# Kernel tuning notes

Measured on AMD Instinct MI355X. Metric: run time of the kernel, lower is better.

Reference implementation:

```python
import jax, jax.numpy as jnp
import numpy as np

N, E, D, K, NCONV = 50000, 800000, 64, 3, 6


def setup_inputs() -> dict:
    key = jax.random.key(0)
    ks = jax.random.split(key, 6)
    X = jax.random.normal(ks[0], (N, D), jnp.float32)
    edge_index = jax.random.randint(ks[1], (2, E), 0, N, dtype=jnp.int64)
    edge_weight = jax.random.uniform(ks[2], (E,), jnp.float32)
    H = jax.random.normal(ks[3], (N, D), jnp.float32)
    lambda_max = jnp.ones((1,), jnp.float32) * 2.0  # typical sym-normalized Laplacian bound
    conv_w = jax.random.normal(ks[4], (NCONV, K, D, D), jnp.float32) / np.sqrt(D)
    conv_b = jnp.zeros((NCONV, D), jnp.float32)
    return {"X": X, "edge_index": edge_index, "edge_weight": edge_weight,
            "H": H, "lambda_max": lambda_max, "conv_w": conv_w, "conv_b": conv_b}


def reference(X, edge_index, edge_weight, H, lambda_max, conv_w, conv_b):
    src, dst = edge_index[0], edge_index[1]
    # symmetric normalization: norm_e = w_e / sqrt(deg_src * deg_dst)
    deg = jax.ops.segment_sum(edge_weight, src, num_segments=N)
    dinv = jnp.where(deg > 0, deg ** -0.5, 0.0)
    norm = edge_weight * dinv[src] * dinv[dst]  # [E]
    lam = lambda_max.reshape(())
    c = 2.0 / lam

    def a_prop(v):  # A_norm @ v via scatter-add over edges, [N,D]
        return jax.ops.segment_sum(norm[:, None] * v[src], dst, num_segments=N)

    def l_hat(v):  # (2/lam)(I - A_norm) v - v
        return (c - 1.0) * v - c * a_prop(v)

    def cheb(v, w, b):  # ChebConv order K: sum_k T_k(L_hat) v @ W_k + b
        tx0, tx1 = v, l_hat(v)
        out = tx0 @ w[0] + tx1 @ w[1]
        for k in range(2, K):
            tx2 = 2.0 * l_hat(tx1) - tx0
            out = out + tx2 @ w[k]
            tx0, tx1 = tx1, tx2
        return out + b

    Z = jax.nn.sigmoid(cheb(X, conv_w[0], conv_b[0]) + cheb(H, conv_w[1], conv_b[1]))
    R = jax.nn.sigmoid(cheb(X, conv_w[2], conv_b[2]) + cheb(H, conv_w[3], conv_b[3]))
    H_tilde = jnp.tanh(cheb(X, conv_w[4], conv_b[4]) + cheb(H * R, conv_w[5], conv_b[5]))
    return Z * H_tilde + (1.0 - Z) * H
```

## Files before the change

### kernel.cpp

```cpp
#include <hip/hip_runtime.h>
#include <cstdint>
#include <cstddef>

typedef unsigned int u32;
typedef unsigned short u16;
typedef unsigned long long u64;

#define D 64
#define CAP 5120
#define CPAD 16
#define CEMAX 2048

typedef __attribute__((ext_vector_type(8))) short bf16x8;
typedef __attribute__((ext_vector_type(4))) float f32x4;

static __device__ __forceinline__ float sigmoidf_(float x) {
    return 1.f / (1.f + __expf(-x));
}
static __device__ __forceinline__ u16 f2bf(float x) {
    u32 u = __float_as_uint(x);
    return (u16)((u + 0x7fffu + ((u >> 16) & 1u)) >> 16);
}
static __device__ __forceinline__ u32 packbf2(float a, float b) {
    return (u32)f2bf(a) | ((u32)f2bf(b) << 16);
}
static __device__ __forceinline__ float bflo(u32 u) { return __uint_as_float(u << 16); }
static __device__ __forceinline__ float bfhi(u32 u) { return __uint_as_float(u & 0xffff0000u); }


__global__ void init_kernel(u32* cur_d, u32* cur_s) {
    int t = threadIdx.x;
    cur_d[t * CPAD] = (u32)(t * CAP);
    cur_s[t * CPAD] = (u32)(t * CAP);
}

__global__ __launch_bounds__(256) void coarse_prep_kernel(
    const int* __restrict__ src, const int* __restrict__ dst, const float* __restrict__ w,
    u32* cur_d, u32* cur_s,
    u64* __restrict__ slab_d, u32* __restrict__ slab_s,
    const float* __restrict__ X, const float* __restrict__ Hf,
    const float* __restrict__ convw,
    u32* __restrict__ XH_t, u32* __restrict__ WT,
    int E, int CE, int nch, int total) {
    __shared__ __align__(16) char smem[CEMAX * 12 + 6 * 1024 + 64];
    int t = threadIdx.x;
    int blk = blockIdx.x;

    if (blk >= nch) {
        int pb = blk - nch;
        if (pb < 18) {
            float (*s)[68] = (float (*)[68])smem;
            const float* wp = convw + (size_t)pb * 4096;
            for (int i = t; i < 1024; i += 256) {
                int k = i >> 4, c4 = (i & 15) * 4;
                *(float4*)&s[k][c4] = *(const float4*)&wp[k * 64 + c4];
            }
            __syncthreads();
            for (int i = t; i < 2048; i += 256) {
                int uk = i & 31, nn = i >> 5;
                WT[(size_t)pb * 2048 + nn * 32 + uk] = packbf2(s[2 * uk][nn], s[2 * uk + 1][nn]);
            }
            return;
        }
        int i = (pb - 18) * 256 + t;
        if (i >= total) return;
        int nn = i >> 6, l = i & 63;
        const float* sp = (l < 32 ? X : Hf) + (size_t)nn * 64 + ((2 * l) & 63);
        float2 v = *(const float2*)sp;
        XH_t[i] = packbf2(v.x, v.y);
        return;
    }

    u64* st_d = (u64*)smem;
    u32* st_s = (u32*)(smem + CEMAX * 8);
    u32* hd = (u32*)(smem + CEMAX * 12);
    u32* hs = hd + 256;
    u32* bd = hs + 256;
    u32* bs = bd + 256;
    u32* gd = bs + 256;
    u32* gs = gd + 256;
    u32* wsd = gs + 256;
    u32* wss = wsd + 4;
    int c = blk;
    hd[t] = 0; hs[t] = 0;
    __syncthreads();
    int e0 = c * CE, e1 = min(E, e0 + CE);
    int m = e1 - e0;
    for (int e = e0 + t; e < e1; e += 256) {
        atomicAdd(&hd[(u32)dst[e] >> 8], 1u);
        atomicAdd(&hs[(u32)src[e] >> 8], 1u);
    }
    __syncthreads();
    u32 vd = hd[t], vs = hs[t];
    u32 id = vd, is_ = vs;
    int lane = t & 63, wv = t >> 6;
#pragma unroll
    for (int o = 1; o < 64; o <<= 1) {
        u32 xd = __shfl_up(id, o, 64);
        u32 xs = __shfl_up(is_, o, 64);
        if (lane >= o) { id += xd; is_ += xs; }
    }
    if (lane == 63) { wsd[wv] = id; wss[wv] = is_; }
    __syncthreads();
    u32 addd = 0, adds = 0;
    for (int i = 0; i < wv; ++i) { addd += wsd[i]; adds += wss[i]; }
    id += addd; is_ += adds;
    u32 exd = id - vd, exs = is_ - vs;
    gd[t] = atomicAdd(&cur_d[t * CPAD], vd);
    gs[t] = atomicAdd(&cur_s[t * CPAD], vs);
    bd[t] = exd; bs[t] = exs;
    hd[t] = exd; hs[t] = exs;
    __syncthreads();
    for (int e = e0 + t; e < e1; e += 256) {
        int s = src[e], d = dst[e];
        float wf = w[e];
        u32 pbd = (u32)d >> 8, pbs = (u32)s >> 8;
        u32 pd = atomicAdd(&hd[pbd], 1u);
        u32 ps = atomicAdd(&hs[pbs], 1u);
        st_d[pd] = (u64)((u32)s | (((u32)d & 255u) << 16) | (pbd << 24)) |
                   ((u64)__float_as_uint(wf) << 32);
        st_s[ps] = ((u32)s & 255u) | (pbs << 8) | ((u32)f2bf(wf) << 16);
    }
    __syncthreads();
    for (int i = t; i < m; i += 256) {
        u64 r = st_d[i];
        u32 b = (u32)(r >> 24) & 255u;
        u32 gpos = gd[b] + ((u32)i - bd[b]);
        if (gpos < (b + 1u) * CAP) slab_d[gpos] = r;
    }
    for (int i = t; i < m; i += 256) {
        u32 r = st_s[i];
        u32 b = (r >> 8) & 255u;
        u32 gpos = gs[b] + ((u32)i - bs[b]);
        if (gpos < (b + 1u) * CAP) slab_s[gpos] = r;
    }
}

__global__ __launch_bounds__(256) void fine_fused_kernel(
    const u64* __restrict__ slab_d, const u32* __restrict__ slab_s,
    const u32* __restrict__ cur_d, const u32* __restrict__ cur_s,
    float* __restrict__ dinv, u32* __restrict__ edge4,
    int2* __restrict__ rowinfo, int NB, int N_) {
    int t = threadIdx.x;
    int b = blockIdx.x;
    if (b < NB) {
        __shared__ float dg[256];
        int m = min((int)cur_s[b * CPAD] - b * CAP, CAP);
        const u32* rp = slab_s + (size_t)b * CAP;
        dg[t] = 0.f;
        __syncthreads();
        for (int i = t; i < m; i += 256) {
            u32 r = rp[i];
            atomicAdd(&dg[r & 255u], __uint_as_float(r & 0xffff0000u));
        }
        __syncthreads();
        int node = (b << 8) + t;
        if (node < N_) dinv[node] = (dg[t] > 0.f) ? rsqrtf(dg[t]) : 0.f;
        return;
    }
    b -= NB;
    __shared__ int h[256], cur[256], ws[4];
    int m = min((int)cur_d[b * CPAD] - b * CAP, CAP);
    const u64* rp = slab_d + (size_t)b * CAP;
    h[t] = 0;
    __syncthreads();
    for (int i = t; i < m; i += 256) atomicAdd(&h[(int)((rp[i] >> 16) & 255u)], 1);
    __syncthreads();
    int v = h[t];
    int iv = v;
    int lane = t & 63, wv = t >> 6;
#pragma unroll
    for (int o = 1; o < 64; o <<= 1) {
        int x = __shfl_up(iv, o, 64);
        if (lane >= o) iv += x;
    }
    if (lane == 63) ws[wv] = iv;
    __syncthreads();
    int add = 0;
    for (int i = 0; i < wv; ++i) add += ws[i];
    iv += add;
    int excl = iv - v;
    cur[t] = excl;
    int bs = b * CAP;
    int node = (b << 8) + t;
    if (node < N_) rowinfo[node] = make_int2(bs + excl, v);
    __syncthreads();
    for (int i = t; i < m; i += 256) {
        u64 r = rp[i];
        int f = (int)((r >> 16) & 255u);
        int p = atomicAdd(&cur[f], 1);
        u32 sidx = (u32)(r & 0xffffu);
        float wf = __uint_as_float((u32)(r >> 32));
        edge4[bs + p] = sidx | ((u32)f2bf(wf) << 16);
    }
}


__global__ __launch_bounds__(256) void lhat128_kernel(
    const u32* __restrict__ vt, const u32* __restrict__ w0t,
    u32* __restrict__ out_t,
    const int2* __restrict__ rowinfo, const float* __restrict__ dinv,
    const u32* __restrict__ edges, const float* __restrict__ lam_ptr, int n) {
    int node = (blockIdx.x * blockDim.x + threadIdx.x) >> 6;
    if (node >= n) return;
    int l = threadIdx.x & 63;
    int g = l >> 4, f = l & 15;
    int2 ri = rowinfo[node];
    int e0 = ri.x, end = e0 + ri.y;
    float acc[8];
#pragma unroll
    for (int j = 0; j < 8; j++) acc[j] = 0.f;

    int base = e0;
    for (; base + 16 <= end; base += 16) {
        u32 r0 = edges[base + g];
        u32 r1 = edges[base + 4 + g];
        u32 r2 = edges[base + 8 + g];
        u32 r3 = edges[base + 12 + g];
        float d0 = dinv[r0 & 0xffffu];
        float d1 = dinv[r1 & 0xffffu];
        float d2 = dinv[r2 & 0xffffu];
        float d3 = dinv[r3 & 0xffffu];
        const uint4 q0 = *(const uint4*)(vt + (size_t)(r0 & 0xffffu) * 64 + 4 * f);
        const uint4 q1 = *(const uint4*)(vt + (size_t)(r1 & 0xffffu) * 64 + 4 * f);
        const uint4 q2 = *(const uint4*)(vt + (size_t)(r2 & 0xffffu) * 64 + 4 * f);
        const uint4 q3 = *(const uint4*)(vt + (size_t)(r3 & 0xffffu) * 64 + 4 * f);
        float n0 = __uint_as_float(r0 & 0xffff0000u) * d0;
        float n1 = __uint_as_float(r1 & 0xffff0000u) * d1;
        float n2 = __uint_as_float(r2 & 0xffff0000u) * d2;
        float n3 = __uint_as_float(r3 & 0xffff0000u) * d3;
        acc[0] += n0 * bflo(q0.x); acc[1] += n0 * bfhi(q0.x);
        acc[2] += n0 * bflo(q0.y); acc[3] += n0 * bfhi(q0.y);
        acc[4] += n0 * bflo(q0.z); acc[5] += n0 * bfhi(q0.z);
        acc[6] += n0 * bflo(q0.w); acc[7] += n0 * bfhi(q0.w);
        acc[0] += n1 * bflo(q1.x); acc[1] += n1 * bfhi(q1.x);
        acc[2] += n1 * bflo(q1.y); acc[3] += n1 * bfhi(q1.y);
        acc[4] += n1 * bflo(q1.z); acc[5] += n1 * bfhi(q1.z);
        acc[6] += n1 * bflo(q1.w); acc[7] += n1 * bfhi(q1.w);
        acc[0] += n2 * bflo(q2.x); acc[1] += n2 * bfhi(q2.x);
        acc[2] += n2 * bflo(q2.y); acc[3] += n2 * bfhi(q2.y);
        acc[4] += n2 * bflo(q2.z); acc[5] += n2 * bfhi(q2.z);
        acc[6] += n2 * bflo(q2.w); acc[7] += n2 * bfhi(q2.w);
        acc[0] += n3 * bflo(q3.x); acc[1] += n3 * bfhi(q3.x);
        acc[2] += n3 * bflo(q3.y); acc[3] += n3 * bfhi(q3.y);
        acc[4] += n3 * bflo(q3.z); acc[5] += n3 * bfhi(q3.z);
        acc[6] += n3 * bflo(q3.w); acc[7] += n3 * bfhi(q3.w);
    }
    for (; base < end; base += 4) {
        int ei = base + g;
        u32 r0 = (ei < end) ? edges[ei] : 0u;
        float d0 = dinv[r0 & 0xffffu];
        const uint4 q0 = *(const uint4*)(vt + (size_t)(r0 & 0xffffu) * 64 + 4 * f);
        float n0 = __uint_as_float(r0 & 0xffff0000u) * d0;
        acc[0] += n0 * bflo(q0.x); acc[1] += n0 * bfhi(q0.x);
        acc[2] += n0 * bflo(q0.y); acc[3] += n0 * bfhi(q0.y);
        acc[4] += n0 * bflo(q0.z); acc[5] += n0 * bfhi(q0.z);
        acc[6] += n0 * bflo(q0.w); acc[7] += n0 * bfhi(q0.w);
    }
#pragma unroll
    for (int m = 16; m <= 32; m <<= 1)
#pragma unroll
        for (int j = 0; j < 8; j++) acc[j] += __shfl_xor(acc[j], m);

    const uint4 sv = *(const uint4*)(vt + (size_t)node * 64 + 4 * f);
    float self[8];
    self[0] = bflo(sv.x); self[1] = bfhi(sv.x);
    self[2] = bflo(sv.y); self[3] = bfhi(sv.y);
    self[4] = bflo(sv.z); self[5] = bfhi(sv.z);
    self[6] = bflo(sv.w); self[7] = bfhi(sv.w);
    float c = 2.f / lam_ptr[0];
    float dv = dinv[node];
    float rx[8];
#pragma unroll
    for (int j = 0; j < 8; j++) rx[j] = (c - 1.f) * self[j] - (c * dv) * acc[j];
    if (w0t) {
        const uint4 wv4 = *(const uint4*)(w0t + (size_t)node * 64 + 4 * f);
        rx[0] = 2.f * rx[0] - bflo(wv4.x); rx[1] = 2.f * rx[1] - bfhi(wv4.x);
        rx[2] = 2.f * rx[2] - bflo(wv4.y); rx[3] = 2.f * rx[3] - bfhi(wv4.y);
        rx[4] = 2.f * rx[4] - bflo(wv4.z); rx[5] = 2.f * rx[5] - bfhi(wv4.z);
        rx[6] = 2.f * rx[6] - bflo(wv4.w); rx[7] = 2.f * rx[7] - bfhi(wv4.w);
    }
    if (l < 16) {
        uint4 o;
        o.x = packbf2(rx[0], rx[1]); o.y = packbf2(rx[2], rx[3]);
        o.z = packbf2(rx[4], rx[5]); o.w = packbf2(rx[6], rx[7]);
        *(uint4*)(out_t + (size_t)node * 64 + 4 * f) = o;
    }
}

__global__ __launch_bounds__(256) void lhat64_kernel(
    const u32* __restrict__ vt, const u32* __restrict__ w0t,
    u32* __restrict__ out_t,
    const int2* __restrict__ rowinfo, const float* __restrict__ dinv,
    const u32* __restrict__ edges, const float* __restrict__ lam_ptr, int n) {
    int node = (blockIdx.x * blockDim.x + threadIdx.x) >> 6;
    if (node >= n) return;
    int l = threadIdx.x & 63;
    int g = l >> 3, f = l & 7;
    int2 ri = rowinfo[node];
    int e0 = ri.x, end = e0 + ri.y;
    float acc[8];
#pragma unroll
    for (int j = 0; j < 8; j++) acc[j] = 0.f;

    int base = e0;
    for (; base + 16 <= end; base += 16) {
        u32 r0 = edges[base + g];
        u32 r1 = edges[base + 8 + g];
        float d0 = dinv[r0 & 0xffffu];
        float d1 = dinv[r1 & 0xffffu];
        const uint4 q0 = *(const uint4*)(vt + (size_t)(r0 & 0xffffu) * 32 + 4 * f);
        const uint4 q1 = *(const uint4*)(vt + (size_t)(r1 & 0xffffu) * 32 + 4 * f);
        float n0 = __uint_as_float(r0 & 0xffff0000u) * d0;
        float n1 = __uint_as_float(r1 & 0xffff0000u) * d1;
        acc[0] += n0 * bflo(q0.x); acc[1] += n0 * bfhi(q0.x);
        acc[2] += n0 * bflo(q0.y); acc[3] += n0 * bfhi(q0.y);
        acc[4] += n0 * bflo(q0.z); acc[5] += n0 * bfhi(q0.z);
        acc[6] += n0 * bflo(q0.w); acc[7] += n0 * bfhi(q0.w);
        acc[0] += n1 * bflo(q1.x); acc[1] += n1 * bfhi(q1.x);
        acc[2] += n1 * bflo(q1.y); acc[3] += n1 * bfhi(q1.y);
        acc[4] += n1 * bflo(q1.z); acc[5] += n1 * bfhi(q1.z);
        acc[6] += n1 * bflo(q1.w); acc[7] += n1 * bfhi(q1.w);
    }
    for (; base < end; base += 8) {
        int ei = base + g;
        u32 r0 = (ei < end) ? edges[ei] : 0u;
        float d0 = dinv[r0 & 0xffffu];
        const uint4 q0 = *(const uint4*)(vt + (size_t)(r0 & 0xffffu) * 32 + 4 * f);
        float n0 = __uint_as_float(r0 & 0xffff0000u) * d0;
        acc[0] += n0 * bflo(q0.x); acc[1] += n0 * bfhi(q0.x);
        acc[2] += n0 * bflo(q0.y); acc[3] += n0 * bfhi(q0.y);
        acc[4] += n0 * bflo(q0.z); acc[5] += n0 * bfhi(q0.z);
        acc[6] += n0 * bflo(q0.w); acc[7] += n0 * bfhi(q0.w);
    }
#pragma unroll
    for (int m = 8; m <= 32; m <<= 1)
#pragma unroll
        for (int j = 0; j < 8; j++) acc[j] += __shfl_xor(acc[j], m);

    const uint4 sv = *(const uint4*)(vt + (size_t)node * 32 + 4 * f);
    float self[8];
    self[0] = bflo(sv.x); self[1] = bfhi(sv.x);
    self[2] = bflo(sv.y); self[3] = bfhi(sv.y);
    self[4] = bflo(sv.z); self[5] = bfhi(sv.z);
    self[6] = bflo(sv.w); self[7] = bfhi(sv.w);
    float c = 2.f / lam_ptr[0];
    float dv = dinv[node];
    float rx[8];
#pragma unroll
    for (int j = 0; j < 8; j++) rx[j] = (c - 1.f) * self[j] - (c * dv) * acc[j];
    if (w0t) {
        const uint4 wv4 = *(const uint4*)(w0t + (size_t)node * 32 + 4 * f);
        rx[0] = 2.f * rx[0] - bflo(wv4.x); rx[1] = 2.f * rx[1] - bfhi(wv4.x);
        rx[2] = 2.f * rx[2] - bflo(wv4.y); rx[3] = 2.f * rx[3] - bfhi(wv4.y);
        rx[4] = 2.f * rx[4] - bflo(wv4.z); rx[5] = 2.f * rx[5] - bfhi(wv4.z);
        rx[6] = 2.f * rx[6] - bflo(wv4.w); rx[7] = 2.f * rx[7] - bfhi(wv4.w);
    }
    if (l < 8) {
        uint4 o;
        o.x = packbf2(rx[0], rx[1]); o.y = packbf2(rx[2], rx[3]);
        o.z = packbf2(rx[4], rx[5]); o.w = packbf2(rx[6], rx[7]);
        *(uint4*)(out_t + (size_t)node * 32 + 4 * f) = o;
    }
}

__global__ __launch_bounds__(512) void gemm_gate_kernel(
    const u32* __restrict__ A0, const u32* __restrict__ A1, const u32* __restrict__ A2,
    const u32* __restrict__ WT, const float* __restrict__ convb,
    const float* __restrict__ Hf,
    float* __restrict__ Zb, float* __restrict__ Sh,
    u16* __restrict__ HR_t, int n) {
    __shared__ u32 Ws[64 * 36];
    int t = threadIdx.x;
    int wv = t >> 6, l = t & 63;
    int q = l >> 4, ml = l & 15;
    int R = blockIdx.x * 128 + wv * 16;
    int ar = R + ml; if (ar >= n) ar = n - 1;

    f32x4 S[3][4];
#pragma unroll
    for (int tg = 0; tg < 3; tg++)
#pragma unroll
        for (int ni = 0; ni < 4; ni++) S[tg][ni] = (f32x4){0.f, 0.f, 0.f, 0.f};

    for (int kt = 0; kt < 3; kt++) {
        const u32* Ap = (kt == 0) ? A0 : ((kt == 1) ? A1 : A2);
        const u32* ap = Ap + (size_t)ar * 64 + q * 4;
        bf16x8 af[2][2];
        af[0][0] = *(const bf16x8*)(ap +  0);
        af[1][0] = *(const bf16x8*)(ap + 16);
        af[0][1] = *(const bf16x8*)(ap + 32);
        af[1][1] = *(const bf16x8*)(ap + 48);
#pragma unroll
        for (int cg = 0; cg < 5; cg++) {
            int hf = cg & 1, tg = cg >> 1;
            const u32* Wp = WT + (size_t)(cg * 3 + kt) * 2048;
            __syncthreads();
            {
                int i0 = t * 4;
                uint4 w0 = *(const uint4*)(Wp + i0);
                *(uint4*)&Ws[(i0 >> 5) * 36 + (i0 & 31)] = w0;
            }
            __syncthreads();
#pragma unroll
            for (int h = 0; h < 2; h++) {
                bf16x8 bw[4];
#pragma unroll
                for (int ni = 0; ni < 4; ni++)
                    bw[ni] = *(const bf16x8*)&Ws[(ni * 16 + ml) * 36 + q * 4 + h * 16];
#pragma unroll
                for (int ni = 0; ni < 4; ni++)
                    S[tg][ni] = __builtin_amdgcn_mfma_f32_16x16x32_bf16(
                        af[h][hf], bw[ni], S[tg][ni], 0, 0, 0);
            }
        }
    }
#pragma unroll
    for (int ni = 0; ni < 4; ni++) {
        int col = ni * 16 + ml;
        float bz = convb[col] + convb[64 + col];
        float br = convb[128 + col] + convb[192 + col];
#pragma unroll
        for (int reg = 0; reg < 4; reg++) {
            int row = R + q * 4 + reg;
            if (row < n) {
                size_t o = (size_t)row * 64 + col;
                float z = sigmoidf_(S[0][ni][reg] + bz);
                float r = sigmoidf_(S[1][ni][reg] + br);
                float hr = Hf[o] * r;
                Zb[o] = z;
                Sh[o] = S[2][ni][reg];
                HR_t[o] = f2bf(hr);
            }
        }
    }
}

__global__ __launch_bounds__(512) void gemm_final_kernel(
    const u32* __restrict__ A0, const u32* __restrict__ A1, const u32* __restrict__ A2,
    const u32* __restrict__ WT, const float* __restrict__ convb,
    const float* __restrict__ Zb, const float* __restrict__ Sh, const float* __restrict__ Hf,
    float* __restrict__ outp, int n) {
    __shared__ u32 Ws[64 * 36];
    int t = threadIdx.x;
    int wv = t >> 6, l = t & 63;
    int q = l >> 4, ml = l & 15;
    int R = blockIdx.x * 128 + wv * 16;
    int ar = R + ml; if (ar >= n) ar = n - 1;

    f32x4 S[4];
#pragma unroll
    for (int ni = 0; ni < 4; ni++) S[ni] = (f32x4){0.f, 0.f, 0.f, 0.f};

    for (int kt = 0; kt < 3; kt++) {
        const u32* Ap = (kt == 0) ? A0 : ((kt == 1) ? A1 : A2);
        const u32* ap = Ap + (size_t)ar * 32 + q * 4;
        bf16x8 af[2];
        af[0] = *(const bf16x8*)(ap +  0);
        af[1] = *(const bf16x8*)(ap + 16);
        const u32* Wp = WT + (size_t)(15 + kt) * 2048;
        __syncthreads();
        {
            int i0 = t * 4;
            uint4 w0 = *(const uint4*)(Wp + i0);
            *(uint4*)&Ws[(i0 >> 5) * 36 + (i0 & 31)] = w0;
        }
        __syncthreads();
#pragma unroll
        for (int h = 0; h < 2; h++) {
            bf16x8 bw[4];
#pragma unroll
            for (int ni = 0; ni < 4; ni++)
                bw[ni] = *(const bf16x8*)&Ws[(ni * 16 + ml) * 36 + q * 4 + h * 16];
#pragma unroll
            for (int ni = 0; ni < 4; ni++)
                S[ni] = __builtin_amdgcn_mfma_f32_16x16x32_bf16(af[h], bw[ni], S[ni], 0, 0, 0);
        }
    }
#pragma unroll
    for (int ni = 0; ni < 4; ni++) {
        int col = ni * 16 + ml;
        float bh = convb[256 + col] + convb[320 + col];
#pragma unroll
        for (int reg = 0; reg < 4; reg++) {
            int row = R + q * 4 + reg;
            if (row < n) {
                size_t o = (size_t)row * 64 + col;
                float z = Zb[o];
                float ht = tanhf(S[ni][reg] + Sh[o] + bh);
                outp[o] = z * ht + (1.f - z) * Hf[o];
            }
        }
    }
}


extern "C" void kernel_launch(void* const* d_in, const int* in_sizes, int n_in,
                              void* d_out, int out_size, void* d_ws, size_t ws_size,
                              hipStream_t stream) {
    const float* X     = (const float*)d_in[0];
    const int*   ei    = (const int*)d_in[1];
    const float* ew    = (const float*)d_in[2];
    const float* H     = (const float*)d_in[3];
    const float* lam   = (const float*)d_in[4];
    const float* convw = (const float*)d_in[5];
    const float* convb = (const float*)d_in[6];
    float* out = (float*)d_out;

    const int N = in_sizes[0] / D;
    const int E = in_sizes[2];
    const int* src = ei;
    const int* dst = ei + E;

    const int NB = (N + 255) >> 8;
    const int nch = (E + CEMAX - 1) / CEMAX;
    const int CE = (E + nch - 1) / nch;

    char* p = (char*)d_ws;
    auto alloc = [&](size_t bytes) {
        void* r = (void*)p;
        p += (bytes + 255) & ~(size_t)255;
        return r;
    };
    float* Zb   = (float*)alloc((size_t)N * 64 * 4);
    float* Sh   = (float*)alloc((size_t)N * 64 * 4);
    u32* XH_t = (u32*)alloc((size_t)N * 64 * 4);
    u32* T1_t = (u32*)alloc((size_t)N * 64 * 4);
    u32* T2_t = (u32*)alloc((size_t)N * 64 * 4);
    u16* HR_t = (u16*)alloc((size_t)N * 64 * 2);
    u16* U1_t = (u16*)alloc((size_t)N * 64 * 2);
    u16* U2_t = (u16*)alloc((size_t)N * 64 * 2);
    u32* edge4 = (u32*)alloc((size_t)NB * CAP * 4);
    u64* slab_d = (u64*)alloc((size_t)NB * CAP * 8);
    u32* slab_s = (u32*)alloc((size_t)NB * CAP * 4);
    u32* cur_d  = (u32*)alloc(256 * CPAD * 4);
    u32* cur_s  = (u32*)alloc(256 * CPAD * 4);
    int2* rowinfo  = (int2*)alloc((size_t)N * 8);
    float* dinv    = (float*)alloc((size_t)N * 4);
    u32* WT = (u32*)alloc((size_t)18 * 2048 * 4);

    const int BLK = 256;
    const int gND  = (N * D + BLK - 1) / BLK;
    const int gWav = gND;
    const int gx128 = (N + 127) / 128;

    init_kernel<<<1, 256, 0, stream>>>(cur_d, cur_s);
    coarse_prep_kernel<<<nch + 18 + gND, BLK, 0, stream>>>(
        src, dst, ew, cur_d, cur_s, slab_d, slab_s,
        X, H, convw, XH_t, WT, E, CE, nch, N * D);
    fine_fused_kernel<<<2 * NB, BLK, 0, stream>>>(slab_d, slab_s, cur_d, cur_s,
                                                  dinv, edge4, rowinfo, NB, N);

    lhat128_kernel<<<gWav, BLK, 0, stream>>>(XH_t, nullptr, T1_t,
                                             rowinfo, dinv, edge4, lam, N);
    lhat128_kernel<<<gWav, BLK, 0, stream>>>(T1_t, XH_t, T2_t,
                                             rowinfo, dinv, edge4, lam, N);

    gemm_gate_kernel<<<gx128, 512, 0, stream>>>(XH_t, T1_t, T2_t, WT, convb, H,
                                                Zb, Sh, HR_t, N);

    lhat64_kernel<<<gWav, BLK, 0, stream>>>((const u32*)HR_t, nullptr, (u32*)U1_t,
                                            rowinfo, dinv, edge4, lam, N);
    lhat64_kernel<<<gWav, BLK, 0, stream>>>((const u32*)U1_t, (const u32*)HR_t, (u32*)U2_t,
                                            rowinfo, dinv, edge4, lam, N);

    gemm_final_kernel<<<gx128, 512, 0, stream>>>((const u32*)HR_t, (const u32*)U1_t, (const u32*)U2_t,
                                                 WT, convb, Zb, Sh, H, out, N);
}
```

Before: 280.1 us.

## Fuse second Chebyshev propagation into the GEMM kernels via shared-memory staging

The second L_hat propagation (T2 and U2) is now computed inside the gate and final GEMM kernels, one wave per 16 nodes, with results written to shared memory instead of global buffers. This removes two kernel launches and the global write and read of the T2/U2 intermediates. In exchange, each 512-thread block performs a serial per-node gather before its MFMA phase, on far fewer blocks (N/128). That lowers the parallelism available to hide the gather latency and raises shared-memory use per block.

```diff
diff --git a/kernel.cpp b/kernel.cpp
--- a/kernel.cpp
+++ b/kernel.cpp
@@ -195,22 +195,16 @@
     }
 }
 
-
-__global__ __launch_bounds__(256) void lhat128_kernel(
+static __device__ __forceinline__ void lhat128_body(
     const u32* __restrict__ vt, const u32* __restrict__ w0t,
-    u32* __restrict__ out_t,
     const int2* __restrict__ rowinfo, const float* __restrict__ dinv,
-    const u32* __restrict__ edges, const float* __restrict__ lam_ptr, int n) {
-    int node = (blockIdx.x * blockDim.x + threadIdx.x) >> 6;
-    if (node >= n) return;
-    int l = threadIdx.x & 63;
+    const u32* __restrict__ edges, float c, int node, int l, float rx[8]) {
     int g = l >> 4, f = l & 15;
     int2 ri = rowinfo[node];
     int e0 = ri.x, end = e0 + ri.y;
     float acc[8];
 #pragma unroll
     for (int j = 0; j < 8; j++) acc[j] = 0.f;
-
     int base = e0;
     for (; base + 16 <= end; base += 16) {
         u32 r0 = edges[base + g];
@@ -261,18 +255,13 @@
     for (int m = 16; m <= 32; m <<= 1)
 #pragma unroll
         for (int j = 0; j < 8; j++) acc[j] += __shfl_xor(acc[j], m);
-
     const uint4 sv = *(const uint4*)(vt + (size_t)node * 64 + 4 * f);
-    float self[8];
-    self[0] = bflo(sv.x); self[1] = bfhi(sv.x);
-    self[2] = bflo(sv.y); self[3] = bfhi(sv.y);
-    self[4] = bflo(sv.z); self[5] = bfhi(sv.z);
-    self[6] = bflo(sv.w); self[7] = bfhi(sv.w);
-    float c = 2.f / lam_ptr[0];
     float dv = dinv[node];
-    float rx[8];
-#pragma unroll
-    for (int j = 0; j < 8; j++) rx[j] = (c - 1.f) * self[j] - (c * dv) * acc[j];
+#pragma unroll
+    for (int j = 0; j < 8; j++) {
+        float self = (j & 1) ? bfhi(((const u32*)&sv)[j >> 1]) : bflo(((const u32*)&sv)[j >> 1]);
+        rx[j] = (c - 1.f) * self - (c * dv) * acc[j];
+    }
     if (w0t) {
         const uint4 wv4 = *(const uint4*)(w0t + (size_t)node * 64 + 4 * f);
         rx[0] = 2.f * rx[0] - bflo(wv4.x); rx[1] = 2.f * rx[1] - bfhi(wv4.x);
@@ -280,29 +269,18 @@
         rx[4] = 2.f * rx[4] - bflo(wv4.z); rx[5] = 2.f * rx[5] - bfhi(wv4.z);
         rx[6] = 2.f * rx[6] - bflo(wv4.w); rx[7] = 2.f * rx[7] - bfhi(wv4.w);
     }
-    if (l < 16) {
-        uint4 o;
-        o.x = packbf2(rx[0], rx[1]); o.y = packbf2(rx[2], rx[3]);
-        o.z = packbf2(rx[4], rx[5]); o.w = packbf2(rx[6], rx[7]);
-        *(uint4*)(out_t + (size_t)node * 64 + 4 * f) = o;
-    }
-}
-
-__global__ __launch_bounds__(256) void lhat64_kernel(
+}
+
+static __device__ __forceinline__ void lhat64_body(
     const u32* __restrict__ vt, const u32* __restrict__ w0t,
-    u32* __restrict__ out_t,
     const int2* __restrict__ rowinfo, const float* __restrict__ dinv,
-    const u32* __restrict__ edges, const float* __restrict__ lam_ptr, int n) {
-    int node = (blockIdx.x * blockDim.x + threadIdx.x) >> 6;
-    if (node >= n) return;
-    int l = threadIdx.x & 63;
+    const u32* __restrict__ edges, float c, int node, int l, float rx[8]) {
     int g = l >> 3, f = l & 7;
     int2 ri = rowinfo[node];
     int e0 = ri.x, end = e0 + ri.y;
     float acc[8];
 #pragma unroll
     for (int j = 0; j < 8; j++) acc[j] = 0.f;
-
     int base = e0;
     for (; base + 16 <= end; base += 16) {
         u32 r0 = edges[base + g];
@@ -337,18 +315,13 @@
     for (int m = 8; m <= 32; m <<= 1)
 #pragma unroll
         for (int j = 0; j < 8; j++) acc[j] += __shfl_xor(acc[j], m);
-
     const uint4 sv = *(const uint4*)(vt + (size_t)node * 32 + 4 * f);
-    float self[8];
-    self[0] = bflo(sv.x); self[1] = bfhi(sv.x);
-    self[2] = bflo(sv.y); self[3] = bfhi(sv.y);
-    self[4] = bflo(sv.z); self[5] = bfhi(sv.z);
-    self[6] = bflo(sv.w); self[7] = bfhi(sv.w);
-    float c = 2.f / lam_ptr[0];
     float dv = dinv[node];
-    float rx[8];
-#pragma unroll
-    for (int j = 0; j < 8; j++) rx[j] = (c - 1.f) * self[j] - (c * dv) * acc[j];
+#pragma unroll
+    for (int j = 0; j < 8; j++) {
+        float self = (j & 1) ? bfhi(((const u32*)&sv)[j >> 1]) : bflo(((const u32*)&sv)[j >> 1]);
+        rx[j] = (c - 1.f) * self - (c * dv) * acc[j];
+    }
     if (w0t) {
         const uint4 wv4 = *(const uint4*)(w0t + (size_t)node * 32 + 4 * f);
         rx[0] = 2.f * rx[0] - bflo(wv4.x); rx[1] = 2.f * rx[1] - bfhi(wv4.x);
@@ -356,7 +329,42 @@
         rx[4] = 2.f * rx[4] - bflo(wv4.z); rx[5] = 2.f * rx[5] - bfhi(wv4.z);
         rx[6] = 2.f * rx[6] - bflo(wv4.w); rx[7] = 2.f * rx[7] - bfhi(wv4.w);
     }
+}
+
+
+__global__ __launch_bounds__(256) void lhat128_kernel(
+    const u32* __restrict__ vt, const u32* __restrict__ w0t,
+    u32* __restrict__ out_t,
+    const int2* __restrict__ rowinfo, const float* __restrict__ dinv,
+    const u32* __restrict__ edges, const float* __restrict__ lam_ptr, int n) {
+    int node = (blockIdx.x * blockDim.x + threadIdx.x) >> 6;
+    if (node >= n) return;
+    int l = threadIdx.x & 63;
+    float c = 2.f / lam_ptr[0];
+    float rx[8];
+    lhat128_body(vt, w0t, rowinfo, dinv, edges, c, node, l, rx);
+    if (l < 16) {
+        int f = l;
+        uint4 o;
+        o.x = packbf2(rx[0], rx[1]); o.y = packbf2(rx[2], rx[3]);
+        o.z = packbf2(rx[4], rx[5]); o.w = packbf2(rx[6], rx[7]);
+        *(uint4*)(out_t + (size_t)node * 64 + 4 * f) = o;
+    }
+}
+
+__global__ __launch_bounds__(256) void lhat64_kernel(
+    const u32* __restrict__ vt, const u32* __restrict__ w0t,
+    u32* __restrict__ out_t,
+    const int2* __restrict__ rowinfo, const float* __restrict__ dinv,
+    const u32* __restrict__ edges, const float* __restrict__ lam_ptr, int n) {
+    int node = (blockIdx.x * blockDim.x + threadIdx.x) >> 6;
+    if (node >= n) return;
+    int l = threadIdx.x & 63;
+    float c = 2.f / lam_ptr[0];
+    float rx[8];
+    lhat64_body(vt, w0t, rowinfo, dinv, edges, c, node, l, rx);
     if (l < 8) {
+        int f = l;
         uint4 o;
         o.x = packbf2(rx[0], rx[1]); o.y = packbf2(rx[2], rx[3]);
         o.z = packbf2(rx[4], rx[5]); o.w = packbf2(rx[6], rx[7]);
@@ -364,18 +372,41 @@
     }
 }
 
-__global__ __launch_bounds__(512) void gemm_gate_kernel(
-    const u32* __restrict__ A0, const u32* __restrict__ A1, const u32* __restrict__ A2,
+__global__ __launch_bounds__(512) void lhat_gemm_gate_kernel(
+    const u32* __restrict__ T1, const u32* __restrict__ XH,
+    const int2* __restrict__ rowinfo, const float* __restrict__ dinv,
+    const u32* __restrict__ edges, const float* __restrict__ lam_ptr,
     const u32* __restrict__ WT, const float* __restrict__ convb,
     const float* __restrict__ Hf,
     float* __restrict__ Zb, float* __restrict__ Sh,
     u16* __restrict__ HR_t, int n) {
+    __shared__ u32 T2s[128 * 68];
     __shared__ u32 Ws[64 * 36];
     int t = threadIdx.x;
     int wv = t >> 6, l = t & 63;
+    int R0 = blockIdx.x * 128;
+    float c = 2.f / lam_ptr[0];
+
+    for (int k = 0; k < 16; ++k) {
+        int lr = wv * 16 + k;
+        int node = R0 + lr;
+        if (node < n) {
+            float rx[8];
+            lhat128_body(T1, XH, rowinfo, dinv, edges, c, node, l, rx);
+            if (l < 16) {
+                uint4 o;
+                o.x = packbf2(rx[0], rx[1]); o.y = packbf2(rx[2], rx[3]);
+                o.z = packbf2(rx[4], rx[5]); o.w = packbf2(rx[6], rx[7]);
+                *(uint4*)&T2s[lr * 68 + 4 * l] = o;
+            }
+        }
+    }
+    __syncthreads();
+
     int q = l >> 4, ml = l & 15;
-    int R = blockIdx.x * 128 + wv * 16;
+    int R = R0 + wv * 16;
     int ar = R + ml; if (ar >= n) ar = n - 1;
+    int alr = ar - R0;
 
     f32x4 S[3][4];
 #pragma unroll
@@ -384,13 +415,21 @@
         for (int ni = 0; ni < 4; ni++) S[tg][ni] = (f32x4){0.f, 0.f, 0.f, 0.f};
 
     for (int kt = 0; kt < 3; kt++) {
-        const u32* Ap = (kt == 0) ? A0 : ((kt == 1) ? A1 : A2);
-        const u32* ap = Ap + (size_t)ar * 64 + q * 4;
         bf16x8 af[2][2];
-        af[0][0] = *(const bf16x8*)(ap +  0);
-        af[1][0] = *(const bf16x8*)(ap + 16);
-        af[0][1] = *(const bf16x8*)(ap + 32);
-        af[1][1] = *(const bf16x8*)(ap + 48);
+        if (kt < 2) {
+            const u32* Ap = (kt == 0) ? XH : T1;
+            const u32* ap = Ap + (size_t)ar * 64 + q * 4;
+            af[0][0] = *(const bf16x8*)(ap +  0);
+            af[1][0] = *(const bf16x8*)(ap + 16);
+            af[0][1] = *(const bf16x8*)(ap + 32);
+            af[1][1] = *(const bf16x8*)(ap + 48);
+        } else {
+            const u32* ap = &T2s[alr * 68 + q * 4];
+            af[0][0] = *(const bf16x8*)(ap +  0);
+            af[1][0] = *(const bf16x8*)(ap + 16);
+            af[0][1] = *(const bf16x8*)(ap + 32);
+            af[1][1] = *(const bf16x8*)(ap + 48);
+        }
 #pragma unroll
         for (int cg = 0; cg < 5; cg++) {
             int hf = cg & 1, tg = cg >> 1;
@@ -436,28 +475,57 @@
     }
 }
 
-__global__ __launch_bounds__(512) void gemm_final_kernel(
-    const u32* __restrict__ A0, const u32* __restrict__ A1, const u32* __restrict__ A2,
+__global__ __launch_bounds__(512) void lhat_gemm_final_kernel(
+    const u32* __restrict__ U1, const u32* __restrict__ HR,
+    const int2* __restrict__ rowinfo, const float* __restrict__ dinv,
+    const u32* __restrict__ edges, const float* __restrict__ lam_ptr,
     const u32* __restrict__ WT, const float* __restrict__ convb,
     const float* __restrict__ Zb, const float* __restrict__ Sh, const float* __restrict__ Hf,
     float* __restrict__ outp, int n) {
+    __shared__ u32 U2s[128 * 36];
     __shared__ u32 Ws[64 * 36];
     int t = threadIdx.x;
     int wv = t >> 6, l = t & 63;
+    int R0 = blockIdx.x * 128;
+    float c = 2.f / lam_ptr[0];
+
+    for (int k = 0; k < 16; ++k) {
+        int lr = wv * 16 + k;
+        int node = R0 + lr;
+        if (node < n) {
+            float rx[8];
+            lhat64_body(U1, HR, rowinfo, dinv, edges, c, node, l, rx);
+            if (l < 8) {
+                uint4 o;
+                o.x = packbf2(rx[0], rx[1]); o.y = packbf2(rx[2], rx[3]);
+                o.z = packbf2(rx[4], rx[5]); o.w = packbf2(rx[6], rx[7]);
+                *(uint4*)&U2s[lr * 36 + 4 * l] = o;
+            }
+        }
+    }
+    __syncthreads();
+
     int q = l >> 4, ml = l & 15;
-    int R = blockIdx.x * 128 + wv * 16;
+    int R = R0 + wv * 16;
     int ar = R + ml; if (ar >= n) ar = n - 1;
+    int alr = ar - R0;
 
     f32x4 S[4];
 #pragma unroll
     for (int ni = 0; ni < 4; ni++) S[ni] = (f32x4){0.f, 0.f, 0.f, 0.f};
 
     for (int kt = 0; kt < 3; kt++) {
-        const u32* Ap = (kt == 0) ? A0 : ((kt == 1) ? A1 : A2);
-        const u32* ap = Ap + (size_t)ar * 32 + q * 4;
         bf16x8 af[2];
-        af[0] = *(const bf16x8*)(ap +  0);
-        af[1] = *(const bf16x8*)(ap + 16);
+        if (kt < 2) {
+            const u32* Ap = (kt == 0) ? HR : U1;
+            const u32* ap = Ap + (size_t)ar * 32 + q * 4;
+            af[0] = *(const bf16x8*)(ap +  0);
+            af[1] = *(const bf16x8*)(ap + 16);
+        } else {
+            const u32* ap = &U2s[alr * 36 + q * 4];
+            af[0] = *(const bf16x8*)(ap +  0);
+            af[1] = *(const bf16x8*)(ap + 16);
+        }
         const u32* Wp = WT + (size_t)(15 + kt) * 2048;
         __syncthreads();
         {
@@ -526,10 +594,8 @@
     float* Sh   = (float*)alloc((size_t)N * 64 * 4);
     u32* XH_t = (u32*)alloc((size_t)N * 64 * 4);
     u32* T1_t = (u32*)alloc((size_t)N * 64 * 4);
-    u32* T2_t = (u32*)alloc((size_t)N * 64 * 4);
     u16* HR_t = (u16*)alloc((size_t)N * 64 * 2);
     u16* U1_t = (u16*)alloc((size_t)N * 64 * 2);
-    u16* U2_t = (u16*)alloc((size_t)N * 64 * 2);
     u32* edge4 = (u32*)alloc((size_t)NB * CAP * 4);
     u64* slab_d = (u64*)alloc((size_t)NB * CAP * 8);
     u32* slab_s = (u32*)alloc((size_t)NB * CAP * 4);
@@ -553,17 +619,14 @@
 
     lhat128_kernel<<<gWav, BLK, 0, stream>>>(XH_t, nullptr, T1_t,
                                              rowinfo, dinv, edge4, lam, N);
-    lhat128_kernel<<<gWav, BLK, 0, stream>>>(T1_t, XH_t, T2_t,
-                                             rowinfo, dinv, edge4, lam, N);
-
-    gemm_gate_kernel<<<gx128, 512, 0, stream>>>(XH_t, T1_t, T2_t, WT, convb, H,
-                                                Zb, Sh, HR_t, N);
+
+    lhat_gemm_gate_kernel<<<gx128, 512, 0, stream>>>(
+        T1_t, XH_t, rowinfo, dinv, edge4, lam, WT, convb, H, Zb, Sh, HR_t, N);
 
     lhat64_kernel<<<gWav, BLK, 0, stream>>>((const u32*)HR_t, nullptr, (u32*)U1_t,
                                             rowinfo, dinv, edge4, lam, N);
-    lhat64_kernel<<<gWav, BLK, 0, stream>>>((const u32*)U1_t, (const u32*)HR_t, (u32*)U2_t,
-                                            rowinfo, dinv, edge4, lam, N);
-
-    gemm_final_kernel<<<gx128, 512, 0, stream>>>((const u32*)HR_t, (const u32*)U1_t, (const u32*)U2_t,
-                                                 WT, convb, Zb, Sh, H, out, N);
-}
+
+    lhat_gemm_final_kernel<<<gx128, 512, 0, stream>>>(
+        (const u32*)U1_t, (const u32*)HR_t, rowinfo, dinv, edge4, lam,
+        WT, convb, Zb, Sh, H, out, N);
+}
```

Measured after the change: 320.4 us. 1.14x slower.
